# Kernel optimization log

Measured on AMD Instinct MI355X. Metric: run time of the kernel, lower is better.

## Reference

```python
import jax, jax.numpy as jnp
import numpy as np

NUM_HEADS = 4
LN_EPS = 1e-5


def setup_inputs() -> dict:
    key = jax.random.key(0)
    ks = jax.random.split(key, 12)
    B, S, D = 8, 2048, 256
    Dh = D // NUM_HEADS
    s = 0.02
    return {
        "descriptors": jax.random.normal(ks[0], (B, S, D), jnp.float32),
        # cached rotary embedding (cos, sin) pair broadcastable over heads
        "keypoints": jax.random.normal(ks[1], (2, B, 1, S, Dh), jnp.float32),
        "Wqkv_w": jax.random.normal(ks[2], (3 * D, D), jnp.float32) * s,
        "Wqkv_b": jax.random.normal(ks[3], (3 * D,), jnp.float32) * s,
        "Wo_w": jax.random.normal(ks[4], (D, D), jnp.float32) * s,
        "Wo_b": jax.random.normal(ks[5], (D,), jnp.float32) * s,
        "W1_w": jax.random.normal(ks[6], (2 * D, 2 * D), jnp.float32) * s,
        "W1_b": jax.random.normal(ks[7], (2 * D,), jnp.float32) * s,
        "ln_g": jnp.ones((2 * D,), jnp.float32),
        "ln_b": jnp.zeros((2 * D,), jnp.float32),
        "W2_w": jax.random.normal(ks[8], (D, 2 * D), jnp.float32) * s,
        "W2_b": jax.random.normal(ks[9], (D,), jnp.float32) * s,
    }


def _rotate_half(x):
    # pairwise rotation: (x0,x1,x2,x3,...) -> (-x1,x0,-x3,x2,...)
    xr = x.reshape(x.shape[:-1] + (x.shape[-1] // 2, 2))
    return jnp.stack((-xr[..., 1], xr[..., 0]), axis=-1).reshape(x.shape)


def reference(descriptors, keypoints, Wqkv_w, Wqkv_b, Wo_w, Wo_b,
              W1_w, W1_b, ln_g, ln_b, W2_w, W2_b):
    B, S, D = descriptors.shape
    H = NUM_HEADS
    Dh = D // H
    # fused QKV projection; torch layout: last dim = (H, Dh, 3) interleaved
    qkv = descriptors @ Wqkv_w.T + Wqkv_b           # [B,S,3D]
    qkv = qkv.reshape(B, S, H, Dh, 3).transpose(0, 2, 1, 3, 4)  # [B,H,S,Dh,3]
    q, k, v = qkv[..., 0], qkv[..., 1], qkv[..., 2]
    # rotary embedding on q, k
    cos, sin = keypoints[0], keypoints[1]           # [B,1,S,Dh]
    q = q * cos + _rotate_half(q) * sin
    k = k * cos + _rotate_half(k) * sin
    # scaled dot-product attention
    scale = jnp.float32(Dh) ** -0.5
    sim = jnp.einsum('bhid,bhjd->bhij', q, k) * scale
    attn = jax.nn.softmax(sim, axis=-1)
    ctx = jnp.einsum('bhij,bhjd->bhid', attn, v)    # [B,H,S,Dh]
    ctx = ctx.transpose(0, 2, 1, 3).reshape(B, S, D)
    message = ctx @ Wo_w.T + Wo_b
    # FFN over concat(descriptors, message)
    x = jnp.concatenate([descriptors, message], axis=-1)  # [B,S,2D]
    x = x @ W1_w.T + W1_b
    mu = jnp.mean(x, axis=-1, keepdims=True)
    var = jnp.var(x, axis=-1, keepdims=True)
    x = (x - mu) * jax.lax.rsqrt(var + LN_EPS) * ln_g + ln_b
    x = jax.nn.gelu(x, approximate=False)
    x = x @ W2_w.T + W2_b
    return descriptors + x
```

## Files before the change

kernel.cpp:

```cpp
#include <hip/hip_runtime.h>
#include <math.h>

#define B_  8
#define S_  2048
#define D_  256
#define H_  4
#define DH  64
#define M_  (B_ * S_)
#define QS  4194304

typedef __attribute__((ext_vector_type(8))) short bf16x8;
typedef __attribute__((ext_vector_type(4))) float f32x4;
typedef unsigned short u16;

#define AS1 __attribute__((address_space(1)))
#define AS3 __attribute__((address_space(3)))

__device__ __forceinline__ u16 f2bf(float x) {
    union { float f; unsigned int u; } c; c.f = x;
    unsigned int r = (c.u + 0x7fffu + ((c.u >> 16) & 1u)) >> 16;
    return (u16)r;
}

__device__ __forceinline__ void gload16(const void* g, void* l) {
    __builtin_amdgcn_global_load_lds((const AS1 unsigned int*)g,
                                     (AS3 unsigned int*)l, 16, 0, 0);
}

__global__ __launch_bounds__(256) void cast_kernel(
    const float* __restrict__ s, u16* __restrict__ d)
{
    const int i = (blockIdx.x * 256 + threadIdx.x) * 4;
    const float4 v = *(const float4*)(s + i);
    u16 o[4] = {f2bf(v.x), f2bf(v.y), f2bf(v.z), f2bf(v.w)};
    *(uint2*)(d + i) = *(const uint2*)o;
}

template <int CONCAT, int RES, int OUTBF16>
__global__ __launch_bounds__(256) void gemm_bf16(
    const u16* __restrict__ A, const u16* __restrict__ A2,
    const u16* __restrict__ W, const float* __restrict__ bias,
    const float* __restrict__ res, float* __restrict__ Cf,
    u16* __restrict__ Cb, int K, int N)
{
    __shared__ u16 As[128 * 64];
    __shared__ u16 Bs[128 * 64];
    const int tid  = threadIdx.x;
    const int w    = tid >> 6;
    const int lane = tid & 63;
    const int n    = lane & 15;
    const int quad = lane >> 4;
    const int m0   = blockIdx.x * 128;
    const int n0   = blockIdx.y * 128;
    const int m_off = (w >> 1) * 64;
    const int n_off = (w & 1) * 64;
    const int lrow = lane >> 3;
    const int lcol = (lane & 7) * 8;

    f32x4 acc[4][4];
#pragma unroll
    for (int i = 0; i < 4; i++)
#pragma unroll
        for (int j = 0; j < 4; j++) acc[i][j] = (f32x4){0.f, 0.f, 0.f, 0.f};

    for (int k0 = 0; k0 < K; k0 += 64) {
        const u16* Asrc;
        int kb, lda;
        if (CONCAT) { Asrc = (k0 < 256) ? A : A2; kb = k0 & 255; lda = 256; }
        else        { Asrc = A; kb = k0; lda = K; }

        __syncthreads();
#pragma unroll
        for (int it = 0; it < 4; it++) {
            const int r0 = it * 32 + w * 8;
            gload16(Asrc + (size_t)(m0 + r0 + lrow) * lda + kb + lcol, &As[r0 * 64]);
            gload16(W    + (size_t)(n0 + r0 + lrow) * K   + k0 + lcol, &Bs[r0 * 64]);
        }
        __syncthreads();

        bf16x8 af[4][2], bf[4][2];
#pragma unroll
        for (int mt = 0; mt < 4; mt++)
#pragma unroll
            for (int t = 0; t < 2; t++)
                af[mt][t] = *(const bf16x8*)&As[(m_off + mt * 16 + n) * 64 + t * 32 + quad * 8];
#pragma unroll
        for (int nt = 0; nt < 4; nt++)
#pragma unroll
            for (int t = 0; t < 2; t++)
                bf[nt][t] = *(const bf16x8*)&Bs[(n_off + nt * 16 + n) * 64 + t * 32 + quad * 8];

#pragma unroll
        for (int mt = 0; mt < 4; mt++)
#pragma unroll
            for (int nt = 0; nt < 4; nt++) {
                acc[mt][nt] = __builtin_amdgcn_mfma_f32_16x16x32_bf16(af[mt][0], bf[nt][0], acc[mt][nt], 0, 0, 0);
                acc[mt][nt] = __builtin_amdgcn_mfma_f32_16x16x32_bf16(af[mt][1], bf[nt][1], acc[mt][nt], 0, 0, 0);
            }
    }

#pragma unroll
    for (int nt = 0; nt < 4; nt++) {
        const int col = n0 + n_off + nt * 16 + n;
        const float bv = bias[col];
#pragma unroll
        for (int mt = 0; mt < 4; mt++) {
#pragma unroll
            for (int r = 0; r < 4; r++) {
                const int row = m0 + m_off + mt * 16 + quad * 4 + r;
                float o = acc[mt][nt][r] + bv;
                if (RES) o += res[(size_t)row * N + col];
                if (OUTBF16) Cb[(size_t)row * N + col] = f2bf(o);
                else         Cf[(size_t)row * N + col] = o;
            }
        }
    }
}

__global__ __launch_bounds__(256) void rope_kernel(
    const float* __restrict__ qkv, const float* __restrict__ kp,
    u16* __restrict__ q, u16* __restrict__ k, u16* __restrict__ v)
{
    const int m = blockIdx.x;
    const int b = m >> 11;
    const int s = m & 2047;
    const float* row = qkv + (size_t)m * 768;
#pragma unroll
    for (int i = 0; i < 3; i++) {
        const int idx = i * 256 + threadIdx.x;
        const int h = idx / 192;
        const int r = idx - h * 192;
        const int d = r / 3;
        const int c = r - d * 3;
        const float val  = row[idx];
        const size_t oidx = ((size_t)(b * H_ + h) * S_ + s) * DH + d;
        if (c == 2) {
            v[oidx] = f2bf(val);
        } else {
            const float pair = row[h * 192 + (d ^ 1) * 3 + c];
            const float rot  = (d & 1) ? pair : -pair;
            const size_t kidx = ((size_t)b * S_ + s) * DH + d;
            const float cs = kp[kidx];
            const float sn = kp[(size_t)B_ * S_ * DH + kidx];
            const float out = val * cs + rot * sn;
            if (c == 0) q[oidx] = f2bf(out * 0.125f);
            else        k[oidx] = f2bf(out);
        }
    }
}

__global__ __launch_bounds__(256) void vtrans_kernel(
    const u16* __restrict__ v, u16* __restrict__ vt)
{
    const int bh = blockIdx.x;
    const int s  = blockIdx.y * 256 + threadIdx.x;
    const u16* src = v + ((size_t)bh * S_ + s) * DH;
    u16* dst = vt + (size_t)bh * DH * S_ + s;
#pragma unroll
    for (int g = 0; g < 8; g++) {
        const uint4 vv = *(const uint4*)(src + g * 8);
        const u16* us = (const u16*)&vv;
#pragma unroll
        for (int i = 0; i < 8; i++) dst[(size_t)(g * 8 + i) * S_] = us[i];
    }
}

__global__ __launch_bounds__(256, 4) void attn_kernel(
    const u16* __restrict__ q, const u16* __restrict__ k,
    const u16* __restrict__ vt, u16* __restrict__ ctx)
{
    __shared__ u16 ks[128 * 64];
    __shared__ u16 vs[64 * 128];
    __shared__ u16 qs[64 * 64];

    const int tid  = threadIdx.x;
    const int w    = tid >> 6;
    const int lane = tid & 63;
    const int n    = lane & 15;
    const int quad = lane >> 4;
    const int lrow = lane >> 3;
    const int vrow = lane >> 4;
    const int bh   = blockIdx.x;
    const int q0   = blockIdx.y * 64;
    const int b    = bh >> 2;
    const int h    = bh & 3;
    const int nsw  = n & 7;

    const int kcol  = (((lane & 7) ^ lrow) * 8);
    const int vcol0 = (((lane & 15) ^ vrow) * 8);
    const int vcol1 = (((lane & 15) ^ (4 + vrow)) * 8);

    const u16* qbase = q  + (size_t)bh * S_ * DH;
    const u16* kbase = k  + (size_t)bh * S_ * DH;
    const u16* vbase = vt + (size_t)bh * DH * S_;

#pragma unroll
    for (int it = 0; it < 2; it++) {
        const int idx = it * 256 + tid;
        const int row = idx >> 3;
        const int c8  = idx & 7;
        *(uint4*)&qs[row * 64 + ((c8 ^ (row & 7)) * 8)] =
            *(const uint4*)(qbase + (size_t)(q0 + row) * DH + c8 * 8);
    }
    __syncthreads();

    bf16x8 qf[2];
    qf[0] = *(const bf16x8*)&qs[(16 * w + n) * 64 + ((quad       ^ nsw) * 8)];
    qf[1] = *(const bf16x8*)&qs[(16 * w + n) * 64 + (((4 + quad) ^ nsw) * 8)];

    f32x4 o[4];
#pragma unroll
    for (int j = 0; j < 4; j++) o[j] = (f32x4){0.f, 0.f, 0.f, 0.f};
    float lrun[4] = {0.f, 0.f, 0.f, 0.f};

    for (int kb = 0; kb < S_ / 128; kb++) {
        const int k0 = kb * 128;
        __syncthreads();
#pragma unroll
        for (int it = 0; it < 4; it++) {
            const int r0 = w * 32 + it * 8;
            gload16(kbase + (size_t)(k0 + r0 + lrow) * DH + kcol, &ks[r0 * 64]);
            const int d0 = w * 16 + it * 4;
            gload16(vbase + (size_t)(d0 + vrow) * S_ + k0 + ((it & 1) ? vcol1 : vcol0),
                    &vs[d0 * 128]);
        }
        __syncthreads();

        f32x4 sacc[8];
#pragma unroll
        for (int j = 0; j < 8; j++) sacc[j] = (f32x4){0.f, 0.f, 0.f, 0.f};
#pragma unroll
        for (int t = 0; t < 2; t++) {
#pragma unroll
            for (int j = 0; j < 8; j++) {
                const bf16x8 kf = *(const bf16x8*)
                    &ks[(16 * j + n) * 64 + (((t * 4 + quad) ^ nsw) * 8)];
                sacc[j] = __builtin_amdgcn_mfma_f32_16x16x32_bf16(qf[t], kf, sacc[j], 0, 0, 0);
            }
        }
        __syncthreads();

#pragma unroll
        for (int r = 0; r < 4; r++) {
            float rs = 0.f;
            const int rw8  = (quad * 4 + r) & 7;
            const int prow = (16 * w + quad * 4 + r) * 128;
#pragma unroll
            for (int j = 0; j < 8; j++) {
                const float p = __expf(sacc[j][r] - 12.f);
                rs += p;
                ks[prow + (((2 * j + (n >> 3)) ^ rw8) * 8) + (n & 7)] = f2bf(p);
            }
            rs += __shfl_xor(rs, 1);
            rs += __shfl_xor(rs, 2);
            rs += __shfl_xor(rs, 4);
            rs += __shfl_xor(rs, 8);
            lrun[r] += rs;
        }

#pragma unroll
        for (int kt = 0; kt < 4; kt++) {
            const bf16x8 pf = *(const bf16x8*)
                &ks[(16 * w + n) * 128 + (((kt * 4 + quad) ^ nsw) * 8)];
#pragma unroll
            for (int nt = 0; nt < 4; nt++) {
                const bf16x8 vf = *(const bf16x8*)
                    &vs[(16 * nt + n) * 128 + (((kt * 4 + quad) ^ nsw) * 8)];
                o[nt] = __builtin_amdgcn_mfma_f32_16x16x32_bf16(pf, vf, o[nt], 0, 0, 0);
            }
        }
    }

#pragma unroll
    for (int r = 0; r < 4; r++) {
        const float inv = 1.f / lrun[r];
        const int row = q0 + 16 * w + quad * 4 + r;
#pragma unroll
        for (int nt = 0; nt < 4; nt++)
            ctx[((size_t)b * S_ + row) * D_ + h * DH + 16 * nt + n] = f2bf(o[nt][r] * inv);
    }
}

__global__ __launch_bounds__(256) void ln_gelu_kernel(
    const float* __restrict__ x, const float* __restrict__ g,
    const float* __restrict__ bt, u16* __restrict__ y)
{
    __shared__ float ss[4], sqs[4];
    const int m = blockIdx.x;
    const float* row = x + (size_t)m * 512;
    const int t = threadIdx.x;
    const float v0 = row[t];
    const float v1 = row[t + 256];
    float s  = v0 + v1;
    float sq = v0 * v0 + v1 * v1;
#pragma unroll
    for (int off = 1; off < 64; off <<= 1) {
        s  += __shfl_xor(s, off);
        sq += __shfl_xor(sq, off);
    }
    const int w = t >> 6;
    if ((t & 63) == 0) { ss[w] = s; sqs[w] = sq; }
    __syncthreads();
    s  = ss[0] + ss[1] + ss[2] + ss[3];
    sq = sqs[0] + sqs[1] + sqs[2] + sqs[3];
    const float mu   = s * (1.f / 512.f);
    const float var  = sq * (1.f / 512.f) - mu * mu;
    const float rstd = rsqrtf(var + 1e-5f);

    const float y0 = (v0 - mu) * rstd * g[t] + bt[t];
    const float y1 = (v1 - mu) * rstd * g[t + 256] + bt[t + 256];
    y[(size_t)m * 512 + t]       = f2bf(0.5f * y0 * (1.f + erff(y0 * 0.70710678118654752f)));
    y[(size_t)m * 512 + t + 256] = f2bf(0.5f * y1 * (1.f + erff(y1 * 0.70710678118654752f)));
}

extern "C" void kernel_launch(void* const* d_in, const int* in_sizes, int n_in,
                              void* d_out, int out_size, void* d_ws, size_t ws_size,
                              hipStream_t stream)
{
    const float* desc   = (const float*)d_in[0];
    const float* kp     = (const float*)d_in[1];
    const float* Wqkv_w = (const float*)d_in[2];
    const float* Wqkv_b = (const float*)d_in[3];
    const float* Wo_w   = (const float*)d_in[4];
    const float* Wo_b   = (const float*)d_in[5];
    const float* W1_w   = (const float*)d_in[6];
    const float* W1_b   = (const float*)d_in[7];
    const float* ln_g   = (const float*)d_in[8];
    const float* ln_b   = (const float*)d_in[9];
    const float* W2_w   = (const float*)d_in[10];
    const float* W2_b   = (const float*)d_in[11];
    float* out = (float*)d_out;
    float* ws  = (float*)d_ws;

    float* qkv_buf = ws;
    float* x1      = ws;
    u16*   x1b   = (u16*)(ws + 2 * (size_t)QS);
    u16*   qb    = (u16*)(ws + 3 * (size_t)QS);
    u16*   kb    = (u16*)(ws + (size_t)(3.5 * QS));
    u16*   vb    = (u16*)(ws + 4 * (size_t)QS);
    u16*   ctxb  = (u16*)(ws + (size_t)(4.5 * QS));
    u16*   descb = (u16*)(ws + 5 * (size_t)QS);
    u16*   msgb  = (u16*)(ws + (size_t)(5.5 * QS));
    u16*   wpool = (u16*)(ws + 6 * (size_t)QS);
    u16*   vtb   = (u16*)(ws + (size_t)(6.5 * QS));
    u16* wqkvb = wpool;
    u16* wob   = wqkvb + 196608;
    u16* w1b   = wob   + 65536;
    u16* w2b   = w1b   + 262144;

    const dim3 blk(256);

    cast_kernel<<<dim3(QS / 1024), blk, 0, stream>>>(desc, descb);
    cast_kernel<<<dim3(196608 / 1024), blk, 0, stream>>>(Wqkv_w, wqkvb);
    cast_kernel<<<dim3(65536 / 1024), blk, 0, stream>>>(Wo_w, wob);
    cast_kernel<<<dim3(262144 / 1024), blk, 0, stream>>>(W1_w, w1b);
    cast_kernel<<<dim3(131072 / 1024), blk, 0, stream>>>(W2_w, w2b);

    gemm_bf16<0, 0, 0><<<dim3(M_ / 128, 768 / 128), blk, 0, stream>>>(
        descb, nullptr, wqkvb, Wqkv_b, nullptr, qkv_buf, nullptr, 256, 768);

    rope_kernel<<<dim3(M_), blk, 0, stream>>>(qkv_buf, kp, qb, kb, vb);

    vtrans_kernel<<<dim3(B_ * H_, S_ / 256), blk, 0, stream>>>(vb, vtb);

    attn_kernel<<<dim3(B_ * H_, S_ / 64), blk, 0, stream>>>(qb, kb, vtb, ctxb);

    gemm_bf16<0, 0, 1><<<dim3(M_ / 128, 256 / 128), blk, 0, stream>>>(
        ctxb, nullptr, wob, Wo_b, nullptr, nullptr, msgb, 256, 256);

    gemm_bf16<1, 0, 0><<<dim3(M_ / 128, 512 / 128), blk, 0, stream>>>(
        descb, msgb, w1b, W1_b, nullptr, x1, nullptr, 512, 512);

    ln_gelu_kernel<<<dim3(M_), blk, 0, stream>>>(x1, ln_g, ln_b, x1b);

    gemm_bf16<0, 1, 0><<<dim3(M_ / 128, 256 / 128), blk, 0, stream>>>(
        x1b, nullptr, w2b, W2_b, desc, out, nullptr, 512, 256);
}
```

Measured before the change: 293.2 us.

## Emit QKV in bf16, vectorize RoPE, merge casts, narrow N tiles for small GEMMs

The QKV GEMM now writes bf16 instead of fp32. The RoPE kernel is rewritten so each thread handles one even/odd pair with vector loads and stores, which removes the scattered scalar accesses and cuts traffic on the intermediate buffer. The five cast launches are merged into one kernel, and the N=256 GEMMs use 64-wide N tiles so more blocks fill the GPU. Rounding QKV to bf16 before RoPE adds a small precision loss.

```diff
diff --git a/kernel.cpp b/kernel.cpp
--- a/kernel.cpp
+++ b/kernel.cpp
@@ -12,14 +12,19 @@
 typedef __attribute__((ext_vector_type(8))) short bf16x8;
 typedef __attribute__((ext_vector_type(4))) float f32x4;
 typedef unsigned short u16;
+typedef unsigned int   u32;
 
 #define AS1 __attribute__((address_space(1)))
 #define AS3 __attribute__((address_space(3)))
 
 __device__ __forceinline__ u16 f2bf(float x) {
-    union { float f; unsigned int u; } c; c.f = x;
-    unsigned int r = (c.u + 0x7fffu + ((c.u >> 16) & 1u)) >> 16;
+    union { float f; u32 u; } c; c.f = x;
+    u32 r = (c.u + 0x7fffu + ((c.u >> 16) & 1u)) >> 16;
     return (u16)r;
+}
+__device__ __forceinline__ float bf2f(u16 x) {
+    union { u32 u; float f; } c; c.u = ((u32)x) << 16;
+    return c.f;
 }
 
 __device__ __forceinline__ void gload16(const void* g, void* l) {
@@ -27,16 +32,27 @@
                                      (AS3 unsigned int*)l, 16, 0, 0);
 }
 
-__global__ __launch_bounds__(256) void cast_kernel(
-    const float* __restrict__ s, u16* __restrict__ d)
-{
-    const int i = (blockIdx.x * 256 + threadIdx.x) * 4;
+__global__ __launch_bounds__(256) void cast5_kernel(
+    const float* __restrict__ s0, u16* __restrict__ d0,
+    const float* __restrict__ s1, u16* __restrict__ d1,
+    const float* __restrict__ s2, u16* __restrict__ d2,
+    const float* __restrict__ s3, u16* __restrict__ d3,
+    const float* __restrict__ s4, u16* __restrict__ d4)
+{
+    int bid = blockIdx.x;
+    const float* s; u16* d;
+    if      (bid < 4096) { s = s0; d = d0; }
+    else if (bid < 4288) { s = s1; d = d1; bid -= 4096; }
+    else if (bid < 4352) { s = s2; d = d2; bid -= 4288; }
+    else if (bid < 4608) { s = s3; d = d3; bid -= 4352; }
+    else                 { s = s4; d = d4; bid -= 4608; }
+    const int i = (bid * 256 + threadIdx.x) * 4;
     const float4 v = *(const float4*)(s + i);
     u16 o[4] = {f2bf(v.x), f2bf(v.y), f2bf(v.z), f2bf(v.w)};
     *(uint2*)(d + i) = *(const uint2*)o;
 }
 
-template <int CONCAT, int RES, int OUTBF16>
+template <int NT, int CONCAT, int RES, int OUTBF16>
 __global__ __launch_bounds__(256) void gemm_bf16(
     const u16* __restrict__ A, const u16* __restrict__ A2,
     const u16* __restrict__ W, const float* __restrict__ bias,
@@ -44,24 +60,24 @@
     u16* __restrict__ Cb, int K, int N)
 {
     __shared__ u16 As[128 * 64];
-    __shared__ u16 Bs[128 * 64];
+    __shared__ u16 Bs[NT * 32 * 64];
     const int tid  = threadIdx.x;
     const int w    = tid >> 6;
     const int lane = tid & 63;
     const int n    = lane & 15;
     const int quad = lane >> 4;
     const int m0   = blockIdx.x * 128;
-    const int n0   = blockIdx.y * 128;
+    const int n0   = blockIdx.y * (NT * 32);
     const int m_off = (w >> 1) * 64;
-    const int n_off = (w & 1) * 64;
+    const int n_off = (w & 1) * (NT * 16);
     const int lrow = lane >> 3;
     const int lcol = (lane & 7) * 8;
 
-    f32x4 acc[4][4];
+    f32x4 acc[4][NT];
 #pragma unroll
     for (int i = 0; i < 4; i++)
 #pragma unroll
-        for (int j = 0; j < 4; j++) acc[i][j] = (f32x4){0.f, 0.f, 0.f, 0.f};
+        for (int j = 0; j < NT; j++) acc[i][j] = (f32x4){0.f, 0.f, 0.f, 0.f};
 
     for (int k0 = 0; k0 < K; k0 += 64) {
         const u16* Asrc;
@@ -74,18 +90,22 @@
         for (int it = 0; it < 4; it++) {
             const int r0 = it * 32 + w * 8;
             gload16(Asrc + (size_t)(m0 + r0 + lrow) * lda + kb + lcol, &As[r0 * 64]);
-            gload16(W    + (size_t)(n0 + r0 + lrow) * K   + k0 + lcol, &Bs[r0 * 64]);
-        }
-        __syncthreads();
-
-        bf16x8 af[4][2], bf[4][2];
+        }
+#pragma unroll
+        for (int it = 0; it < NT; it++) {
+            const int r0 = it * 32 + w * 8;
+            gload16(W + (size_t)(n0 + r0 + lrow) * K + k0 + lcol, &Bs[r0 * 64]);
+        }
+        __syncthreads();
+
+        bf16x8 af[4][2], bf[NT][2];
 #pragma unroll
         for (int mt = 0; mt < 4; mt++)
 #pragma unroll
             for (int t = 0; t < 2; t++)
                 af[mt][t] = *(const bf16x8*)&As[(m_off + mt * 16 + n) * 64 + t * 32 + quad * 8];
 #pragma unroll
-        for (int nt = 0; nt < 4; nt++)
+        for (int nt = 0; nt < NT; nt++)
 #pragma unroll
             for (int t = 0; t < 2; t++)
                 bf[nt][t] = *(const bf16x8*)&Bs[(n_off + nt * 16 + n) * 64 + t * 32 + quad * 8];
@@ -93,14 +113,14 @@
 #pragma unroll
         for (int mt = 0; mt < 4; mt++)
 #pragma unroll
-            for (int nt = 0; nt < 4; nt++) {
+            for (int nt = 0; nt < NT; nt++) {
                 acc[mt][nt] = __builtin_amdgcn_mfma_f32_16x16x32_bf16(af[mt][0], bf[nt][0], acc[mt][nt], 0, 0, 0);
                 acc[mt][nt] = __builtin_amdgcn_mfma_f32_16x16x32_bf16(af[mt][1], bf[nt][1], acc[mt][nt], 0, 0, 0);
             }
     }
 
 #pragma unroll
-    for (int nt = 0; nt < 4; nt++) {
+    for (int nt = 0; nt < NT; nt++) {
         const int col = n0 + n_off + nt * 16 + n;
         const float bv = bias[col];
 #pragma unroll
@@ -118,35 +138,38 @@
 }
 
 __global__ __launch_bounds__(256) void rope_kernel(
-    const float* __restrict__ qkv, const float* __restrict__ kp,
+    const u16* __restrict__ qkv, const float* __restrict__ kp,
     u16* __restrict__ q, u16* __restrict__ k, u16* __restrict__ v)
 {
-    const int m = blockIdx.x;
-    const int b = m >> 11;
-    const int s = m & 2047;
-    const float* row = qkv + (size_t)m * 768;
-#pragma unroll
-    for (int i = 0; i < 3; i++) {
-        const int idx = i * 256 + threadIdx.x;
-        const int h = idx / 192;
-        const int r = idx - h * 192;
-        const int d = r / 3;
-        const int c = r - d * 3;
-        const float val  = row[idx];
-        const size_t oidx = ((size_t)(b * H_ + h) * S_ + s) * DH + d;
-        if (c == 2) {
-            v[oidx] = f2bf(val);
-        } else {
-            const float pair = row[h * 192 + (d ^ 1) * 3 + c];
-            const float rot  = (d & 1) ? pair : -pair;
-            const size_t kidx = ((size_t)b * S_ + s) * DH + d;
-            const float cs = kp[kidx];
-            const float sn = kp[(size_t)B_ * S_ * DH + kidx];
-            const float out = val * cs + rot * sn;
-            if (c == 0) q[oidx] = f2bf(out * 0.125f);
-            else        k[oidx] = f2bf(out);
-        }
-    }
+    const int row = blockIdx.x * 2 + (threadIdx.x >> 7);
+    const int t   = threadIdx.x & 127;
+    const int b   = row >> 11;
+    const int s   = row & 2047;
+    const int h   = t >> 5;
+    const int dp  = t & 31;
+    const int d   = dp * 2;
+
+    const u16* src = qkv + (size_t)row * 768 + h * 192 + dp * 6;
+    const u32 w0 = *(const u32*)(src);
+    const u32 w1 = *(const u32*)(src + 2);
+    const u32 w2 = *(const u32*)(src + 4);
+    const float qe = bf2f((u16)w0), ke = bf2f((u16)(w0 >> 16));
+    const float qo = bf2f((u16)(w1 >> 16));
+    const float ko = bf2f((u16)w2);
+
+    const size_t kidx = ((size_t)b * S_ + s) * DH + d;
+    const float2 cs = *(const float2*)(kp + kidx);
+    const float2 sn = *(const float2*)(kp + (size_t)B_ * S_ * DH + kidx);
+
+    const float qe2 = (qe * cs.x - qo * sn.x) * 0.125f;
+    const float qo2 = (qo * cs.y + qe * sn.y) * 0.125f;
+    const float ke2 = ke * cs.x - ko * sn.x;
+    const float ko2 = ko * cs.y + ke * sn.y;
+
+    const size_t oidx = (((size_t)(b * H_ + h)) * S_ + s) * DH + d;
+    *(u32*)(q + oidx) = (u32)f2bf(qe2) | ((u32)f2bf(qo2) << 16);
+    *(u32*)(k + oidx) = (u32)f2bf(ke2) | ((u32)f2bf(ko2) << 16);
+    *(u32*)(v + oidx) = (w1 & 0xffffu) | (w2 & 0xffff0000u);
 }
 
 __global__ __launch_bounds__(256) void vtrans_kernel(
@@ -332,8 +355,8 @@
     float* out = (float*)d_out;
     float* ws  = (float*)d_ws;
 
-    float* qkv_buf = ws;
-    float* x1      = ws;
+    u16*   qkvb  = (u16*)ws;
+    float* x1    = ws;
     u16*   x1b   = (u16*)(ws + 2 * (size_t)QS);
     u16*   qb    = (u16*)(ws + 3 * (size_t)QS);
     u16*   kb    = (u16*)(ws + (size_t)(3.5 * QS));
@@ -350,29 +373,26 @@
 
     const dim3 blk(256);
 
-    cast_kernel<<<dim3(QS / 1024), blk, 0, stream>>>(desc, descb);
-    cast_kernel<<<dim3(196608 / 1024), blk, 0, stream>>>(Wqkv_w, wqkvb);
-    cast_kernel<<<dim3(65536 / 1024), blk, 0, stream>>>(Wo_w, wob);
-    cast_kernel<<<dim3(262144 / 1024), blk, 0, stream>>>(W1_w, w1b);
-    cast_kernel<<<dim3(131072 / 1024), blk, 0, stream>>>(W2_w, w2b);
-
-    gemm_bf16<0, 0, 0><<<dim3(M_ / 128, 768 / 128), blk, 0, stream>>>(
-        descb, nullptr, wqkvb, Wqkv_b, nullptr, qkv_buf, nullptr, 256, 768);
-
-    rope_kernel<<<dim3(M_), blk, 0, stream>>>(qkv_buf, kp, qb, kb, vb);
+    cast5_kernel<<<dim3(4736), blk, 0, stream>>>(
+        desc, descb, Wqkv_w, wqkvb, Wo_w, wob, W1_w, w1b, W2_w, w2b);
+
+    gemm_bf16<4, 0, 0, 1><<<dim3(M_ / 128, 768 / 128), blk, 0, stream>>>(
+        descb, nullptr, wqkvb, Wqkv_b, nullptr, nullptr, qkvb, 256, 768);
+
+    rope_kernel<<<dim3(M_ / 2), blk, 0, stream>>>(qkvb, kp, qb, kb, vb);
 
     vtrans_kernel<<<dim3(B_ * H_, S_ / 256), blk, 0, stream>>>(vb, vtb);
 
     attn_kernel<<<dim3(B_ * H_, S_ / 64), blk, 0, stream>>>(qb, kb, vtb, ctxb);
 
-    gemm_bf16<0, 0, 1><<<dim3(M_ / 128, 256 / 128), blk, 0, stream>>>(
+    gemm_bf16<2, 0, 0, 1><<<dim3(M_ / 128, 256 / 64), blk, 0, stream>>>(
         ctxb, nullptr, wob, Wo_b, nullptr, nullptr, msgb, 256, 256);
 
-    gemm_bf16<1, 0, 0><<<dim3(M_ / 128, 512 / 128), blk, 0, stream>>>(
+    gemm_bf16<4, 1, 0, 0><<<dim3(M_ / 128, 512 / 128), blk, 0, stream>>>(
         descb, msgb, w1b, W1_b, nullptr, x1, nullptr, 512, 512);
 
     ln_gelu_kernel<<<dim3(M_), blk, 0, stream>>>(x1, ln_g, ln_b, x1b);
 
-    gemm_bf16<0, 1, 0><<<dim3(M_ / 128, 256 / 128), blk, 0, stream>>>(
+    gemm_bf16<2, 0, 1, 0><<<dim3(M_ / 128, 256 / 64), blk, 0, stream>>>(
         x1b, nullptr, w2b, W2_b, desc, out, nullptr, 512, 256);
 }
```

After: 266.7 us. -9.0%, faster.
